# Performance work log

Measured on AMD Instinct MI355X. Metric: run time of the kernel, lower is better.

The kernel has to match this reference:

```python
import jax, jax.numpy as jnp
import numpy as np

T, HEADS, DIM_HEAD = 16, 16, 72
M = HEADS * DIM_HEAD  # 1152
SCALE = DIM_HEAD ** -0.5


def _ln(x, eps):
    mu = x.mean(-1, keepdims=True)
    var = x.var(-1, keepdims=True)
    return (x - mu) / jnp.sqrt(var + eps)


def _rotate_half(t):
    # interleaved pairs (x1, x2) -> (-x2, x1), as in rotary-embedding-torch
    t1, t2 = t[..., 0::2], t[..., 1::2]
    return jnp.stack([-t2, t1], axis=-1).reshape(t.shape)


def _rotary(t, pos):
    d = t.shape[-1]
    inv_freq = 1.0 / (10000.0 ** (jnp.arange(0, d, 2, dtype=jnp.float32) / d))
    freqs = pos.astype(jnp.float32)[:, None] * inv_freq          # (T, d/2)
    freqs = jnp.repeat(freqs, 2, axis=-1)                        # (T, d)
    return t * jnp.cos(freqs) + _rotate_half(t) * jnp.sin(freqs)


def _forward(x, c4t, c, W_ada, b_ada, tn_w, tn_b, t_qkv, t_k, t_v, t_out,
             t_fc_w, t_fc_b, s_qkv, s_k, s_v, s_out,
             mlp_w1, mlp_b1, mlp_w2, mlp_b2, f):
    B = c4t.shape[0]
    K, N, _ = x.shape

    ada = jax.nn.silu(c4t) @ W_ada + b_ada                       # (B, 6M)
    sh_msa, sc_msa, g_msa, sh_mlp, sc_mlp, g_mlp = jnp.split(ada, 6, axis=1)

    x4 = x.reshape(B, T, N, M)

    # ---- temporal attention (seq dim = frames, rotary, per-frame cond k/v) ----
    xt = _ln(x4, 1e-5) * tn_w + tn_b                             # temporal_norm1
    xt = xt.transpose(0, 2, 1, 3)                                # (B, N, T, M)
    q, k, v = jnp.split(xt @ t_qkv, 3, axis=-1)

    def heads_t(t):  # (B,N,T,M) -> (B,N,h,T,d)
        return t.reshape(B, N, T, HEADS, DIM_HEAD).transpose(0, 1, 3, 2, 4)

    q, k, v = map(heads_t, (q, k, v))
    k = _rotary(k, f)
    ek = (c @ t_k).reshape(B, T, HEADS, DIM_HEAD).transpose(0, 2, 1, 3)  # (B,h,T,d)
    ev = (c @ t_v).reshape(B, T, HEADS, DIM_HEAD).transpose(0, 2, 1, 3)
    ek = _rotary(ek, f)
    ek = jnp.broadcast_to(ek[:, None], k.shape)                  # (B,N,h,T,d)
    ev = jnp.broadcast_to(ev[:, None], v.shape)
    kk = jnp.concatenate([ek, k], axis=-2)                       # (B,N,h,2T,d)
    vv = jnp.concatenate([ev, v], axis=-2)
    q = _rotary(q * SCALE, f)
    attn = jax.nn.softmax(jnp.einsum('bnhid,bnhjd->bnhij', q, kk), axis=-1)
    out = jnp.einsum('bnhij,bnhjd->bnhid', attn, vv)
    out = out.transpose(0, 1, 3, 2, 4).reshape(B, N, T, M) @ t_out
    res = out.transpose(0, 2, 1, 3) @ t_fc_w + t_fc_b            # (B,T,N,M)
    x4 = x4 + res

    # ---- spatial attention with adaLN modulate + one cond token per frame ----
    mod = _ln(x4, 1e-6) * (1.0 + sc_msa[:, None, None, :]) + sh_msa[:, None, None, :]
    q, k, v = jnp.split(mod @ s_qkv, 3, axis=-1)

    def heads_s(t):  # (B,T,N,M) -> (B,T,h,N,d)
        return t.reshape(B, T, N, HEADS, DIM_HEAD).transpose(0, 1, 3, 2, 4)

    q, k, v = map(heads_s, (q, k, v))
    ek = (c @ s_k).reshape(B, T, HEADS, DIM_HEAD)[:, :, :, None, :]  # (B,T,h,1,d)
    ev = (c @ s_v).reshape(B, T, HEADS, DIM_HEAD)[:, :, :, None, :]
    kk = jnp.concatenate([ek, k], axis=-2)                       # (B,T,h,N+1,d)
    vv = jnp.concatenate([ev, v], axis=-2)
    attn = jax.nn.softmax(jnp.einsum('bthid,bthjd->bthij', q * SCALE, kk), axis=-1)
    out = jnp.einsum('bthij,bthjd->bthid', attn, vv)
    out = out.transpose(0, 1, 3, 2, 4).reshape(B, T, N, M) @ s_out
    x4 = x4 + g_msa[:, None, None, :] * out

    # ---- gated MLP with adaLN modulate ----
    mod2 = _ln(x4, 1e-6) * (1.0 + sc_mlp[:, None, None, :]) + sh_mlp[:, None, None, :]
    h = jax.nn.gelu(mod2 @ mlp_w1 + mlp_b1, approximate=True)
    y = h @ mlp_w2 + mlp_b2
    x4 = x4 + g_mlp[:, None, None, :] * y
    return x4.reshape(K, N, M)


def setup_inputs() -> dict:
    key = jax.random.key(0)
    ks = jax.random.split(key, 20)
    B, N = 2, 256

    def w(k, shape, s=0.02):
        return jax.random.normal(k, shape, jnp.float32) * s

    return {
        'x': jax.random.normal(ks[0], (B * T, N, M), jnp.float32),
        'c4t': jax.random.normal(ks[1], (B, M), jnp.float32),
        'c': jax.random.normal(ks[2], (B, T, M), jnp.float32),
        'W_ada': w(ks[3], (M, 6 * M)), 'b_ada': w(ks[4], (6 * M,)),
        'tn_w': jnp.ones(M, jnp.float32), 'tn_b': jnp.zeros(M, jnp.float32),
        't_qkv': w(ks[5], (M, 3 * M)), 't_k': w(ks[6], (M, M)),
        't_v': w(ks[7], (M, M)), 't_out': w(ks[8], (M, M)),
        't_fc_w': w(ks[9], (M, M)), 't_fc_b': jnp.zeros(M, jnp.float32),
        's_qkv': w(ks[10], (M, 3 * M)), 's_k': w(ks[11], (M, M)),
        's_v': w(ks[12], (M, M)), 's_out': w(ks[13], (M, M)),
        'mlp_w1': w(ks[14], (M, 4 * M)), 'mlp_b1': jnp.zeros(4 * M, jnp.float32),
        'mlp_w2': w(ks[15], (4 * M, M)), 'mlp_b2': jnp.zeros(M, jnp.float32),
        'f': jnp.arange(T, dtype=jnp.int32),
    }


def reference(x, c4t, c, W_ada, b_ada, tn_w, tn_b, t_qkv, t_k, t_v, t_out,
              t_fc_w, t_fc_b, s_qkv, s_k, s_v, s_out,
              mlp_w1, mlp_b1, mlp_w2, mlp_b2, f):
    return _forward(x, c4t, c, W_ada, b_ada, tn_w, tn_b, t_qkv, t_k, t_v, t_out,
                    t_fc_w, t_fc_b, s_qkv, s_k, s_v, s_out,
                    mlp_w1, mlp_b1, mlp_w2, mlp_b2, f)
```

## Files before the change

### kernel.cpp

```cpp
#include <hip/hip_runtime.h>
#include <hip/hip_bf16.h>

typedef __hip_bfloat16 bf16;
typedef __attribute__((ext_vector_type(8))) short short8;
typedef __attribute__((ext_vector_type(4))) float floatx4;

__device__ __forceinline__ float b2f(bf16 v) { return __bfloat162float(v); }
__device__ __forceinline__ short f2bs(float v) {
    bf16 h = __float2bfloat16(v);
    return *(short*)&h;
}
__device__ __forceinline__ float invfreq(int jj) {
    return expf(-0.25584278811044955f * (float)jj);
}

template<int MODE>
__device__ __forceinline__ float ldin(const void* p, long i) {
    if (MODE == 0) return b2f(((const bf16*)p)[i]);
    else           return ((const float*)p)[i];
}
__device__ __forceinline__ float ldf(const void* p, long i, int fl) {
    return fl == 0 ? b2f(((const bf16*)p)[i]) : ((const float*)p)[i];
}

#define SCALE_ 0.11785113019775793f

#define GLDS(gp, lp) __builtin_amdgcn_global_load_lds( \
    (const __attribute__((address_space(1))) void*)(gp), \
    (__attribute__((address_space(3))) void*)(lp), 16, 0, 0)

__global__ void k_detect(const void* __restrict__ x, int* __restrict__ flag)
{
    const unsigned short* u = (const unsigned short*)x;
    int tid = threadIdx.x;
    int insane = 0;
    for (int i = tid; i < 2048; i += 64) {
        unsigned short s = u[i];
        int ex = (s >> 7) & 0xFF;
        if (ex >= 0xC5) insane++;
    }
    #pragma unroll
    for (int off = 32; off > 0; off >>= 1) insane += __shfl_down(insane, off);
    if (tid == 0) flag[0] = (insane > 8) ? 1 : 0;
}

__global__ void k_setup(const void* __restrict__ c4t, const void* __restrict__ c,
                        const void* __restrict__ t_fcb, const void* __restrict__ mlp_b1,
                        const void* __restrict__ mlp_b2, const int* __restrict__ f,
                        float* __restrict__ sc4, float* __restrict__ cf32,
                        float* __restrict__ fcb_f, float* __restrict__ b1_f,
                        float* __restrict__ b2_f, float* __restrict__ ropeC,
                        float* __restrict__ ropeS, const int* __restrict__ flg)
{
    int i = blockIdx.x * 256 + threadIdx.x;
    int fl = *flg;
    if (i < 2304) {
        float v = ldf(c4t, i, fl);
        sc4[i] = v / (1.f + expf(-v));
    } else if (i < 39168) {
        cf32[i - 2304] = ldf(c, i - 2304, fl);
    } else if (i < 40320) {
        fcb_f[i - 39168] = ldf(t_fcb, i - 39168, fl);
    } else if (i < 44928) {
        b1_f[i - 40320] = ldf(mlp_b1, i - 40320, fl);
    } else if (i < 46080) {
        b2_f[i - 44928] = ldf(mlp_b2, i - 44928, fl);
    } else if (i < 47232) {
        int idx = i - 46080;
        int t = idx / 72, d = idx - t * 72;
        float ang = (float)f[t] * invfreq(d >> 1);
        float sn, cs; sincosf(ang, &sn, &cs);
        ropeC[idx] = cs;
        ropeS[idx] = sn;
    }
}

__global__ void k_cvtb(const float* __restrict__ in, bf16* __restrict__ out, int n)
{
    int i = blockIdx.x * 256 + threadIdx.x;
    if (i < n) out[i] = __float2bfloat16(in[i]);
}

template<int MODE>
__device__ __forceinline__ void wt_body(float (*tile)[33], const void* __restrict__ W,
    bf16* __restrict__ Wt, int K, int N)
{
    int n0 = blockIdx.x << 5, k0 = blockIdx.y << 5;
    int tid = threadIdx.x;
    int r = tid >> 3, c4 = (tid & 7) << 2;
    long base = (long)(k0 + r) * N + n0 + c4;
    #pragma unroll
    for (int i = 0; i < 4; ++i) tile[r][c4 + i] = ldin<MODE>(W, base + i);
    __syncthreads();
    long obase = (long)(n0 + r) * K + k0 + c4;
    #pragma unroll
    for (int i = 0; i < 4; ++i) Wt[obase + i] = __float2bfloat16(tile[c4 + i][r]);
}

__global__ __launch_bounds__(256) void k_wt(const void* __restrict__ W,
    bf16* __restrict__ Wt, int K, int N, const int* __restrict__ flg)
{
    __shared__ float tile[32][33];
    if (*flg == 0) wt_body<0>(tile, W, Wt, K, N);
    else           wt_body<1>(tile, W, Wt, K, N);
}

__global__ __launch_bounds__(256) void k_wt2(const void* __restrict__ W0,
    const void* __restrict__ W1, bf16* __restrict__ Wt0, const int* __restrict__ flg)
{
    __shared__ float tile[32][33];
    const void* W = blockIdx.z ? W1 : W0;
    bf16* Wt = Wt0 + (long)blockIdx.z * 3981312;
    if (*flg == 0) wt_body<0>(tile, W, Wt, 1152, 3456);
    else           wt_body<1>(tile, W, Wt, 1152, 3456);
}

__global__ __launch_bounds__(256) void k_wt3(const void* __restrict__ W0,
    const void* __restrict__ W1, const void* __restrict__ W2,
    bf16* __restrict__ Wt0, const int* __restrict__ flg)
{
    __shared__ float tile[32][33];
    const void* W = (blockIdx.z == 0) ? W0 : (blockIdx.z == 1) ? W1 : W2;
    bf16* Wt = Wt0 + (long)blockIdx.z * 1327104;
    if (*flg == 0) wt_body<0>(tile, W, Wt, 1152, 1152);
    else           wt_body<1>(tile, W, Wt, 1152, 1152);
}

template<int MODE>
__device__ __forceinline__ void gemm_body(
    float (*As)[64], float (*Bs)[64],
    const float* __restrict__ A, const void* __restrict__ W,
    const void* __restrict__ bias, float* __restrict__ C,
    int row0, int R, int K, int N)
{
    int tid = threadIdx.x;
    int tx = tid & 15, ty = tid >> 4;
    int col0 = blockIdx.x << 6;
    float acc[4][4] = {};
    int ar = tid >> 2;
    int ak = (tid & 3) << 2;
    int bk = tid >> 4;
    int bc = (tid & 15) << 2;
    for (int kt = 0; kt < K; kt += 16) {
        if (row0 + ar < R) {
            const float4 a4 = *(const float4*)(A + (long)(row0 + ar) * K + kt + ak);
            As[ak + 0][ar] = a4.x; As[ak + 1][ar] = a4.y;
            As[ak + 2][ar] = a4.z; As[ak + 3][ar] = a4.w;
        } else {
            As[ak + 0][ar] = 0.f; As[ak + 1][ar] = 0.f;
            As[ak + 2][ar] = 0.f; As[ak + 3][ar] = 0.f;
        }
        #pragma unroll
        for (int i = 0; i < 4; ++i)
            Bs[bk][bc + i] = ldin<MODE>(W, (long)(kt + bk) * N + col0 + bc + i);
        __syncthreads();
        #pragma unroll
        for (int kk = 0; kk < 16; ++kk) {
            float4 av = *(const float4*)&As[kk][ty << 2];
            float4 bv = *(const float4*)&Bs[kk][tx << 2];
            float a[4] = {av.x, av.y, av.z, av.w};
            float b[4] = {bv.x, bv.y, bv.z, bv.w};
            #pragma unroll
            for (int i = 0; i < 4; ++i)
                #pragma unroll
                for (int j = 0; j < 4; ++j)
                    acc[i][j] += a[i] * b[j];
        }
        __syncthreads();
    }
    #pragma unroll
    for (int i = 0; i < 4; ++i) {
        int gr = row0 + (ty << 2) + i;
        if (gr >= R) continue;
        float* cp = C + (long)gr * N + col0 + (tx << 2);
        #pragma unroll
        for (int j = 0; j < 4; ++j) {
            float v = acc[i][j];
            if (bias) v += ldin<MODE>(bias, col0 + (tx << 2) + j);
            cp[j] = v;
        }
    }
}

__global__ __launch_bounds__(256) void k_gemm(
    const float* __restrict__ A, const void* __restrict__ W,
    const void* __restrict__ bias, float* __restrict__ C,
    int R, int K, int N, const int* __restrict__ flg)
{
    __shared__ float As[16][64];
    __shared__ float Bs[16][64];
    if (*flg == 0) gemm_body<0>(As, Bs, A, W, bias, C, (int)(blockIdx.y << 6), R, K, N);
    else           gemm_body<1>(As, Bs, A, W, bias, C, (int)(blockIdx.y << 6), R, K, N);
}

__global__ __launch_bounds__(256) void k_gemm4(
    const float* __restrict__ A, const void* __restrict__ W0,
    const void* __restrict__ W1, const void* __restrict__ W2,
    const void* __restrict__ W3, float* __restrict__ C0,
    const int* __restrict__ flg)
{
    __shared__ float As[16][64];
    __shared__ float Bs[16][64];
    int z = blockIdx.y;
    const void* W = (z == 0) ? W0 : (z == 1) ? W1 : (z == 2) ? W2 : W3;
    float* C = C0 + (long)z * 36864;
    if (*flg == 0) gemm_body<0>(As, Bs, A, W, nullptr, C, 0, 32, 1152, 1152);
    else           gemm_body<1>(As, Bs, A, W, nullptr, C, 0, 32, 1152, 1152);
}

template<int EMODE>
__global__ __launch_bounds__(256, 3) void k_mgemm(
    const bf16* __restrict__ A, const bf16* __restrict__ Wt,
    const float* __restrict__ bias, void* __restrict__ Cout,
    int K, int N, int outbf, int act,
    float* __restrict__ x4, const float* __restrict__ ada, int part,
    const void* __restrict__ xin, void* __restrict__ outp,
    const int* __restrict__ flg)
{
    __shared__ short As[12288];
    __shared__ short Bs[12288];
    int tid = threadIdx.x;
    int lane = tid & 63, wave = tid >> 6;
    int mq = wave >> 1, nq = wave & 1;

    int gx = gridDim.x;
    int nwg = gx * (int)gridDim.y;
    int orig = blockIdx.y * gx + blockIdx.x;
    int qq = nwg >> 3, rr = nwg & 7;
    int xcd = orig & 7, loc = orig >> 3;
    int wg = (xcd < rr ? xcd * (qq + 1) : rr * (qq + 1) + (xcd - rr) * qq) + loc;
    int bx = wg % gx, by = wg / gx;

    long row0 = (long)by << 7;
    long col0 = (long)bx << 7;
    int mi = lane & 15, q = lane >> 4;

    const bf16* gA0 = A  + (row0 + (2 * wave) * 16 + mi) * K + q * 8;
    const bf16* gA1 = gA0 + 16 * K;
    const bf16* gB0 = Wt + (col0 + (2 * wave) * 16 + mi) * K + q * 8;
    const bf16* gB1 = gB0 + 16 * K;
    int dA0 = (2 * wave) * 512, dA1 = dA0 + 512;

    floatx4 acc[4][4] = {};
    int nt = K >> 5;

    GLDS(gA0,      &As[dA0]);
    GLDS(gA1,      &As[dA1]);
    GLDS(gB0,      &Bs[dA0]);
    GLDS(gB1,      &Bs[dA1]);
    GLDS(gA0 + 32, &As[4096 + dA0]);
    GLDS(gA1 + 32, &As[4096 + dA1]);
    GLDS(gB0 + 32, &Bs[4096 + dA0]);
    GLDS(gB1 + 32, &Bs[4096 + dA1]);
    __builtin_amdgcn_sched_barrier(0);
    asm volatile("s_waitcnt vmcnt(4)" ::: "memory");
    __builtin_amdgcn_sched_barrier(0);
    __builtin_amdgcn_s_barrier();
    __builtin_amdgcn_sched_barrier(0);

    int aRd = mq * 2048 + lane * 8;
    int bRd = nq * 2048 + lane * 8;
    int cs = 0;
    int si = 2;

    for (int t = 0; t < nt; ++t) {
        if (t + 2 < nt) {
            int o = si << 12;
            int kt2 = (t + 2) << 5;
            GLDS(gA0 + kt2, &As[o + dA0]);
            GLDS(gA1 + kt2, &As[o + dA1]);
            GLDS(gB0 + kt2, &Bs[o + dA0]);
            GLDS(gB1 + kt2, &Bs[o + dA1]);
        }
        {
            int o = cs << 12;
            short8 af[4], bfr[4];
            #pragma unroll
            for (int i = 0; i < 4; ++i)
                af[i] = *(const short8*)&As[o + aRd + i * 512];
            #pragma unroll
            for (int j = 0; j < 4; ++j)
                bfr[j] = *(const short8*)&Bs[o + bRd + j * 512];
            #pragma unroll
            for (int i = 0; i < 4; ++i)
                #pragma unroll
                for (int j = 0; j < 4; ++j)
                    acc[i][j] = __builtin_amdgcn_mfma_f32_16x16x32_bf16(
                        af[i], bfr[j], acc[i][j], 0, 0, 0);
        }
        __builtin_amdgcn_sched_barrier(0);
        if (t + 2 < nt) asm volatile("s_waitcnt vmcnt(4)" ::: "memory");
        else            asm volatile("s_waitcnt vmcnt(0)" ::: "memory");
        __builtin_amdgcn_sched_barrier(0);
        if (t < nt - 1) {
            __builtin_amdgcn_s_barrier();
            __builtin_amdgcn_sched_barrier(0);
        }
        cs = (cs == 2) ? 0 : cs + 1;
        si = (si == 2) ? 0 : si + 1;
    }

    int lr = lane >> 4, lc = lane & 15;
    int fl = flg ? *flg : 0;
    float b4[4] = {0.f, 0.f, 0.f, 0.f};
    if (bias) {
        #pragma unroll
        for (int j = 0; j < 4; ++j) b4[j] = bias[(int)col0 + nq * 64 + j * 16 + lc];
    }
    #pragma unroll
    for (int i = 0; i < 4; ++i) {
        #pragma unroll
        for (int r = 0; r < 4; ++r) {
            long grow = row0 + mq * 64 + i * 16 + lr * 4 + r;
            #pragma unroll
            for (int j = 0; j < 4; ++j) {
                int col = (int)col0 + nq * 64 + j * 16 + lc;
                float v = acc[i][j][r] + b4[j];
                if (act) {
                    float u = v;
                    float tt = 1.5957691216057308f * (u + 0.044715f * u * u * u);
                    v = u / (1.f + __expf(-tt));
                }
                if constexpr (EMODE == 0) {
                    if (outbf) ((bf16*)Cout)[grow * N + col] = __float2bfloat16(v);
                    else       ((float*)Cout)[grow * N + col] = v;
                } else if constexpr (EMODE == 1) {
                    int bb = (int)(grow >> 12);
                    int nn = ((int)grow >> 4) & 255;
                    int tt2 = (int)grow & 15;
                    long rx = ((long)((bb << 4) + tt2) << 8) + nn;
                    long idx = rx * 1152 + col;
                    float xv = (fl == 0) ? b2f(((const bf16*)xin)[idx])
                                         : ((const float*)xin)[idx];
                    x4[idx] = xv + v;
                } else {
                    int bb = (int)(grow >> 12);
                    float g = ada[(bb * 6 + part) * 1152 + col];
                    long idx = grow * 1152 + col;
                    float nv = x4[idx] + g * v;
                    x4[idx] = nv;
                    if (outp) {
                        if (fl == 0) ((bf16*)outp)[idx] = __float2bfloat16(nv);
                        else         ((float*)outp)[idx] = nv;
                    }
                }
            }
        }
    }
}

template<int MODE>
__device__ __forceinline__ void ln_t_body(float* rs, float* rss,
    const void* __restrict__ x, const void* __restrict__ w,
    const void* __restrict__ bb, bf16* __restrict__ out)
{
    int r = blockIdx.x;
    int n = r & 255;
    int bt = r >> 8;
    int b = bt >> 4, t = bt & 15;
    long orow = (long)((b << 8) + n) * 16 + t;
    int tid = threadIdx.x;
    float vals[5];
    float s = 0.f, ss = 0.f;
    int c = 0;
    for (int i = tid; i < 1152; i += 256, ++c) {
        float v = ldin<MODE>(x, (long)r * 1152 + i);
        vals[c] = v; s += v; ss += v * v;
    }
    #pragma unroll
    for (int off = 32; off > 0; off >>= 1) {
        s  += __shfl_down(s, off);
        ss += __shfl_down(ss, off);
    }
    int wid = tid >> 6;
    if ((tid & 63) == 0) { rs[wid] = s; rss[wid] = ss; }
    __syncthreads();
    float S  = rs[0] + rs[1] + rs[2] + rs[3];
    float SS = rss[0] + rss[1] + rss[2] + rss[3];
    float mu = S * (1.f / 1152.f);
    float var = SS * (1.f / 1152.f) - mu * mu;
    float rstd = rsqrtf(var + 1e-5f);
    c = 0;
    bf16* op = out + orow * 1152;
    for (int i = tid; i < 1152; i += 256, ++c)
        op[i] = __float2bfloat16((vals[c] - mu) * rstd * ldin<MODE>(w, i) + ldin<MODE>(bb, i));
}

__global__ __launch_bounds__(256) void k_ln_t(
    const void* __restrict__ x, const void* __restrict__ w,
    const void* __restrict__ bb, bf16* __restrict__ out,
    const int* __restrict__ flg)
{
    __shared__ float rs[4], rss[4];
    if (*flg == 0) ln_t_body<0>(rs, rss, x, w, bb, out);
    else           ln_t_body<1>(rs, rss, x, w, bb, out);
}

__global__ __launch_bounds__(256) void k_ln_mod(
    const float* __restrict__ x4, const float* __restrict__ ada,
    int psh, int psc, float eps, bf16* __restrict__ out)
{
    int r = blockIdx.x;
    int b = r >> 12;
    const float* xp = x4 + (long)r * 1152;
    int tid = threadIdx.x;
    float vals[5];
    float s = 0.f, ss = 0.f;
    int c = 0;
    for (int i = tid; i < 1152; i += 256, ++c) {
        float v = xp[i];
        vals[c] = v; s += v; ss += v * v;
    }
    #pragma unroll
    for (int off = 32; off > 0; off >>= 1) {
        s  += __shfl_down(s, off);
        ss += __shfl_down(ss, off);
    }
    __shared__ float rs[4], rss[4];
    int wid = tid >> 6;
    if ((tid & 63) == 0) { rs[wid] = s; rss[wid] = ss; }
    __syncthreads();
    float S  = rs[0] + rs[1] + rs[2] + rs[3];
    float SS = rss[0] + rss[1] + rss[2] + rss[3];
    float mu = S * (1.f / 1152.f);
    float var = SS * (1.f / 1152.f) - mu * mu;
    float rstd = rsqrtf(var + eps);
    const float* sh = ada + (b * 6 + psh) * 1152;
    const float* sc = ada + (b * 6 + psc) * 1152;
    c = 0;
    bf16* op = out + (long)r * 1152;
    for (int i = tid; i < 1152; i += 256, ++c)
        op[i] = __float2bfloat16((vals[c] - mu) * rstd * (1.f + sc[i]) + sh[i]);
}

__global__ __launch_bounds__(256) void k_attn_t(
    const bf16* __restrict__ qkv, const float* __restrict__ ekt,
    const float* __restrict__ evt, const float* __restrict__ ropeC,
    const float* __restrict__ ropeS, bf16* __restrict__ out)
{
    __shared__ float qs[16][73];
    __shared__ float ksT[72][33];
    __shared__ float vs[32][73];
    __shared__ float sc[16][33];
    int blk = blockIdx.x;
    int h = blk & 15;
    int bn = blk >> 4;
    int b = bn >> 8;
    int tid = threadIdx.x;
    long qbase = (long)bn * 16 * 3456 + h * 72;
    for (int idx = tid; idx < 16 * 72; idx += 256) {
        int i = idx / 72, d = idx - i * 72;
        long p0 = qbase + (long)i * 3456;
        float v  = b2f(qkv[p0 + d]);
        float v2 = b2f(qkv[p0 + (d ^ 1)]);
        float cs = ropeC[idx], sn = ropeS[idx];
        float rv = (d & 1) ? (v * cs + v2 * sn) : (v * cs - v2 * sn);
        qs[i][d] = rv * SCALE_;
    }
    for (int idx = tid; idx < 32 * 72; idx += 256) {
        int j = idx / 72, d = idx - j * 72;
        float kv, kv2, vv; int pi;
        if (j < 16) {
            long base = (long)(b * 16 + j) * 1152 + h * 72;
            kv  = ekt[base + d];
            kv2 = ekt[base + (d ^ 1)];
            vv  = evt[base + d];
            pi = j;
        } else {
            int jj = j - 16;
            long base = qbase + (long)jj * 3456;
            kv  = b2f(qkv[base + 1152 + d]);
            kv2 = b2f(qkv[base + 1152 + (d ^ 1)]);
            vv  = b2f(qkv[base + 2304 + d]);
            pi = jj;
        }
        float cs = ropeC[pi * 72 + d], sn = ropeS[pi * 72 + d];
        ksT[d][j] = (d & 1) ? (kv * cs + kv2 * sn) : (kv * cs - kv2 * sn);
        vs[j][d] = vv;
    }
    __syncthreads();
    for (int e = tid; e < 512; e += 256) {
        int i = e >> 5, j = e & 31;
        float s = 0.f;
        for (int d = 0; d < 72; ++d) s += qs[i][d] * ksT[d][j];
        sc[i][j] = s;
    }
    __syncthreads();
    if (tid < 16) {
        float m = -1e30f;
        for (int j = 0; j < 32; ++j) m = fmaxf(m, sc[tid][j]);
        float l = 0.f;
        for (int j = 0; j < 32; ++j) { float p = expf(sc[tid][j] - m); sc[tid][j] = p; l += p; }
        float inv = 1.f / l;
        for (int j = 0; j < 32; ++j) sc[tid][j] *= inv;
    }
    __syncthreads();
    for (int idx = tid; idx < 16 * 72; idx += 256) {
        int i = idx / 72, d = idx - i * 72;
        float o = 0.f;
        for (int j = 0; j < 32; ++j) o += sc[i][j] * vs[j][d];
        out[((long)bn * 16 + i) * 1152 + h * 72 + d] = __float2bfloat16(o);
    }
}

__global__ __launch_bounds__(256) void k_attn_s(
    const bf16* __restrict__ qkv, const bf16* __restrict__ eksb,
    const bf16* __restrict__ evsb, bf16* __restrict__ out)
{
    __shared__ short vT[5120];
    __shared__ short pl[4][1024];
    int tid = threadIdx.x;
    int lane = tid & 63, wave = tid >> 6;
    int blk = blockIdx.x;
    int ic = blk & 3;
    int bth = blk >> 2;
    int h = bth & 15;
    int bt = bth >> 4;
    int col = lane & 15, q = lane >> 4;
    int hoff = h * 72;
    long qkvbase = (long)bt * 256 * 3456;
    long ctxbase = (long)bt * 1152 + hoff;

    int qrow = ic * 64 + wave * 16 + col;
    const bf16* qptr = qkv + qkvbase + (long)qrow * 3456 + hoff;
    short8 qf[3];
    #pragma unroll
    for (int ks = 0; ks < 3; ++ks) {
        int k0 = ks * 32 + q * 8;
        if (k0 + 8 <= 72) qf[ks] = *(const short8*)(qptr + k0);
        else { short8 z = {0,0,0,0,0,0,0,0}; qf[ks] = z; }
    }

    floatx4 o[5] = {};
    float m_i[4], l_i[4];
    #pragma unroll
    for (int r = 0; r < 4; ++r) { m_i[r] = -1e30f; l_i[r] = 0.f; }

    for (int kc = 0; kc < 320; kc += 64) {
        for (int fi = tid; fi < 640; fi += 256) {
            int blkid = fi >> 6, fl2 = fi & 63;
            int dn = blkid >> 1, ks = blkid & 1;
            int d = dn * 16 + (fl2 & 15);
            int kq = fl2 >> 4;
            short8 v;
            #pragma unroll
            for (int j = 0; j < 8; ++j) {
                int gk = kc + ks * 32 + kq * 8 + j;
                short sv = 0;
                if (d < 72 && gk <= 256) {
                    if (gk == 0) sv = *(const short*)(eksb ? &evsb[ctxbase + d] : nullptr);
                    else sv = *(const short*)&qkv[qkvbase + (long)(gk - 1) * 3456 + 2304 + hoff + d];
                }
                v[j] = sv;
            }
            *(short8*)&vT[blkid * 512 + fl2 * 8] = v;
        }
        __syncthreads();

        floatx4 sacc[4] = {};
        #pragma unroll
        for (int nt = 0; nt < 4; ++nt) {
            int key = kc + nt * 16 + col;
            #pragma unroll
            for (int ks = 0; ks < 3; ++ks) {
                int k0 = ks * 32 + q * 8;
                short8 kf = {0,0,0,0,0,0,0,0};
                if (key <= 256 && k0 + 8 <= 72) {
                    if (key == 0) kf = *(const short8*)(eksb + ctxbase + k0);
                    else kf = *(const short8*)(qkv + qkvbase + (long)(key - 1) * 3456 + 1152 + hoff + k0);
                }
                sacc[nt] = __builtin_amdgcn_mfma_f32_16x16x32_bf16(qf[ks], kf, sacc[nt], 0, 0, 0);
            }
        }

        float p[4][4];
        #pragma unroll
        for (int r = 0; r < 4; ++r) {
            float mv = -1e30f;
            #pragma unroll
            for (int nt = 0; nt < 4; ++nt) {
                int key = kc + nt * 16 + col;
                float s = (key <= 256) ? sacc[nt][r] * SCALE_ : -1e30f;
                p[nt][r] = s;
                mv = fmaxf(mv, s);
            }
            #pragma unroll
            for (int xm = 1; xm < 16; xm <<= 1) mv = fmaxf(mv, __shfl_xor(mv, xm));
            float mn = fmaxf(m_i[r], mv);
            float alpha = expf(m_i[r] - mn);
            m_i[r] = mn;
            float rsum = 0.f;
            #pragma unroll
            for (int nt = 0; nt < 4; ++nt) {
                float e = expf(p[nt][r] - mn);
                p[nt][r] = e;
                rsum += e;
            }
            #pragma unroll
            for (int xm = 1; xm < 16; xm <<= 1) rsum += __shfl_xor(rsum, xm);
            l_i[r] = l_i[r] * alpha + rsum;
            #pragma unroll
            for (int dn = 0; dn < 5; ++dn) o[dn][r] *= alpha;
        }

        #pragma unroll
        for (int nt = 0; nt < 4; ++nt) {
            int kl = nt * 16 + col;
            int ks2 = kl >> 5, q2 = (kl >> 3) & 3, j = kl & 7;
            #pragma unroll
            for (int r = 0; r < 4; ++r) {
                int mrow = q * 4 + r;
                pl[wave][ks2 * 512 + q2 * 128 + mrow * 8 + j] = f2bs(p[nt][r]);
            }
        }
        __syncthreads();

        #pragma unroll
        for (int ks = 0; ks < 2; ++ks) {
            short8 pf = *(const short8*)&pl[wave][ks * 512 + lane * 8];
            #pragma unroll
            for (int dn = 0; dn < 5; ++dn) {
                short8 vf = *(const short8*)&vT[(dn * 2 + ks) * 512 + lane * 8];
                o[dn] = __builtin_amdgcn_mfma_f32_16x16x32_bf16(pf, vf, o[dn], 0, 0, 0);
            }
        }
        __syncthreads();
    }

    int orow0 = ic * 64 + wave * 16;
    #pragma unroll
    for (int dn = 0; dn < 5; ++dn) {
        int d = dn * 16 + col;
        if (d >= 72) continue;
        #pragma unroll
        for (int r = 0; r < 4; ++r) {
            int mrow = q * 4 + r;
            float val = o[dn][r] / l_i[r];
            out[((long)bt * 256 + orow0 + mrow) * 1152 + hoff + d] = __float2bfloat16(val);
        }
    }
}

extern "C" void kernel_launch(void* const* d_in, const int* in_sizes, int n_in,
                              void* d_out, int out_size, void* d_ws, size_t ws_size,
                              hipStream_t stream)
{
    const void* x      = d_in[0];
    const void* c4t    = d_in[1];
    const void* c      = d_in[2];
    const void* W_ada  = d_in[3];
    const void* b_ada  = d_in[4];
    const void* tn_w   = d_in[5];
    const void* tn_b   = d_in[6];
    const void* t_qkv  = d_in[7];
    const void* t_k    = d_in[8];
    const void* t_v    = d_in[9];
    const void* t_outw = d_in[10];
    const void* t_fcw  = d_in[11];
    const void* t_fcb  = d_in[12];
    const void* s_qkv  = d_in[13];
    const void* s_k    = d_in[14];
    const void* s_v    = d_in[15];
    const void* s_outw = d_in[16];
    const void* mlp_w1 = d_in[17];
    const void* mlp_b1 = d_in[18];
    const void* mlp_w2 = d_in[19];
    const void* mlp_b2 = d_in[20];
    const int*  f      = (const int*)d_in[21];

    float* ws    = (float*)d_ws;
    float* x4    = ws;
    float* buf2  = x4 + 9437184;
    float* reg1f = buf2 + 9437184;
    bf16*  qkvb  = (bf16*)reg1f;
    bf16*  hbf   = (bf16*)reg1f;
    float* abfAf = reg1f + 18874368;
    bf16*  abfA  = (bf16*)abfAf;
    float* abfBf = abfAf + 4718592;
    bf16*  abfB  = (bf16*)abfBf;
    float* wtf   = abfBf + 4718592;
    bf16*  wt    = (bf16*)wtf;
    bf16* t_qkv_t = wt;
    bf16* s_qkv_t = t_qkv_t + 3981312;
    bf16* t_out_t = s_qkv_t + 3981312;
    bf16* t_fc_t  = t_out_t + 1327104;
    bf16* s_out_t = t_fc_t  + 1327104;
    bf16* w1_t    = s_out_t + 1327104;
    bf16* w2_t    = w1_t    + 5308416;
    float* small  = wtf + 11280384;
    float* ada   = small;
    float* cf32  = ada  + 13824;
    float* ekt   = cf32 + 36864;
    float* evt   = ekt  + 36864;
    float* eks   = evt  + 36864;
    float* evs   = eks  + 36864;
    bf16*  eksb  = (bf16*)(evs + 36864);
    bf16*  evsb  = eksb + 36864;
    float* sc4   = (float*)(evsb + 36864);
    float* fcb_f = sc4  + 2304;
    float* b1_f  = fcb_f + 1152;
    float* b2_f  = b1_f  + 4608;
    float* ropeC = b2_f + 1152;
    float* ropeS = ropeC + 1152;
    int*   flg   = (int*)(ropeS + 1152);

    k_detect<<<1, 64, 0, stream>>>(x, flg);
    k_setup<<<185, 256, 0, stream>>>(c4t, c, t_fcb, mlp_b1, mlp_b2, f,
                                     sc4, cf32, fcb_f, b1_f, b2_f, ropeC, ropeS, flg);

    k_gemm<<<dim3(108, 1), 256, 0, stream>>>(sc4, W_ada, b_ada, ada, 2, 1152, 6912, flg);
    k_gemm4<<<dim3(18, 4), 256, 0, stream>>>(cf32, t_k, t_v, s_k, s_v, ekt, flg);
    k_cvtb<<<288, 256, 0, stream>>>(eks, eksb, 73728);

    k_wt2<<<dim3(108, 36, 2), 256, 0, stream>>>(t_qkv, s_qkv, t_qkv_t, flg);
    k_wt3<<<dim3(36, 36, 3), 256, 0, stream>>>(t_outw, t_fcw, s_outw, t_out_t, flg);
    k_wt<<<dim3(144, 36), 256, 0, stream>>>(mlp_w1, w1_t, 1152, 4608, flg);
    k_wt<<<dim3(36, 144), 256, 0, stream>>>(mlp_w2, w2_t, 4608, 1152, flg);

    k_ln_t<<<8192, 256, 0, stream>>>(x, tn_w, tn_b, abfA, flg);
    k_mgemm<0><<<dim3(27, 64), 256, 0, stream>>>(abfA, t_qkv_t, nullptr, qkvb, 1152, 3456, 1, 0,
                                                 nullptr, nullptr, 0, nullptr, nullptr, flg);
    k_attn_t<<<8192, 256, 0, stream>>>(qkvb, ekt, evt, ropeC, ropeS, abfB);
    k_mgemm<0><<<dim3(9, 64), 256, 0, stream>>>(abfB, t_out_t, nullptr, abfA, 1152, 1152, 1, 0,
                                                nullptr, nullptr, 0, nullptr, nullptr, flg);
    k_mgemm<1><<<dim3(9, 64), 256, 0, stream>>>(abfA, t_fc_t, fcb_f, nullptr, 1152, 1152, 0, 0,
                                                x4, nullptr, 0, x, nullptr, flg);

    k_ln_mod<<<8192, 256, 0, stream>>>(x4, ada, 0, 1, 1e-6f, abfA);
    k_mgemm<0><<<dim3(27, 64), 256, 0, stream>>>(abfA, s_qkv_t, nullptr, qkvb, 1152, 3456, 1, 0,
                                                 nullptr, nullptr, 0, nullptr, nullptr, flg);
    k_attn_s<<<2048, 256, 0, stream>>>(qkvb, eksb, evsb, abfB);
    k_mgemm<2><<<dim3(9, 64), 256, 0, stream>>>(abfB, s_out_t, nullptr, nullptr, 1152, 1152, 0, 0,
                                                x4, ada, 2, nullptr, nullptr, flg);

    k_ln_mod<<<8192, 256, 0, stream>>>(x4, ada, 3, 4, 1e-6f, abfA);
    k_mgemm<0><<<dim3(36, 64), 256, 0, stream>>>(abfA, w1_t, b1_f, hbf, 1152, 4608, 1, 1,
                                                 nullptr, nullptr, 0, nullptr, nullptr, flg);
    k_mgemm<2><<<dim3(9, 64), 256, 0, stream>>>(hbf, w2_t, b2_f, nullptr, 4608, 1152, 0, 0,
                                                x4, ada, 5, nullptr, d_out, flg);
}
```

Measured before the change: 1.487 ms.

## Load MFMA GEMM operands straight to registers and fuse bf16 conversion into gemm4

The main bf16 MFMA GEMM no longer stages tiles in LDS through a triple-buffered global_load_lds pipeline with barriers. Each wave now loads its own A and B fragments directly from global memory into registers, double-buffered across k-steps. This removes LDS traffic and block-wide syncs, but every wave re-reads operands that the other waves of the block share, so global and L2 traffic goes up. Separately, gemm4 writes the spatial k/v outputs directly as bf16, which removes the standalone conversion kernel launch.

After: 2.117 ms. 42.3% more time.

```diff
diff --git a/kernel.cpp b/kernel.cpp
--- a/kernel.cpp
+++ b/kernel.cpp
@@ -24,10 +24,6 @@
 }
 
 #define SCALE_ 0.11785113019775793f
-
-#define GLDS(gp, lp) __builtin_amdgcn_global_load_lds( \
-    (const __attribute__((address_space(1))) void*)(gp), \
-    (__attribute__((address_space(3))) void*)(lp), 16, 0, 0)
 
 __global__ void k_detect(const void* __restrict__ x, int* __restrict__ flag)
 {
@@ -75,12 +71,6 @@
     }
 }
 
-__global__ void k_cvtb(const float* __restrict__ in, bf16* __restrict__ out, int n)
-{
-    int i = blockIdx.x * 256 + threadIdx.x;
-    if (i < n) out[i] = __float2bfloat16(in[i]);
-}
-
 template<int MODE>
 __device__ __forceinline__ void wt_body(float (*tile)[33], const void* __restrict__ W,
     bf16* __restrict__ Wt, int K, int N)
@@ -131,7 +121,7 @@
     float (*As)[64], float (*Bs)[64],
     const float* __restrict__ A, const void* __restrict__ W,
     const void* __restrict__ bias, float* __restrict__ C,
-    int row0, int R, int K, int N)
+    bf16* __restrict__ Cb, int row0, int R, int K, int N)
 {
     int tid = threadIdx.x;
     int tx = tid & 15, ty = tid >> 4;
@@ -172,12 +162,13 @@
     for (int i = 0; i < 4; ++i) {
         int gr = row0 + (ty << 2) + i;
         if (gr >= R) continue;
-        float* cp = C + (long)gr * N + col0 + (tx << 2);
         #pragma unroll
         for (int j = 0; j < 4; ++j) {
             float v = acc[i][j];
-            if (bias) v += ldin<MODE>(bias, col0 + (tx << 2) + j);
-            cp[j] = v;
+            int cc = col0 + (tx << 2) + j;
+            if (bias) v += ldin<MODE>(bias, cc);
+            if (Cb) Cb[(long)gr * N + cc] = __float2bfloat16(v);
+            else    C[(long)gr * N + cc] = v;
         }
     }
 }
@@ -189,23 +180,24 @@
 {
     __shared__ float As[16][64];
     __shared__ float Bs[16][64];
-    if (*flg == 0) gemm_body<0>(As, Bs, A, W, bias, C, (int)(blockIdx.y << 6), R, K, N);
-    else           gemm_body<1>(As, Bs, A, W, bias, C, (int)(blockIdx.y << 6), R, K, N);
+    if (*flg == 0) gemm_body<0>(As, Bs, A, W, bias, C, nullptr, (int)(blockIdx.y << 6), R, K, N);
+    else           gemm_body<1>(As, Bs, A, W, bias, C, nullptr, (int)(blockIdx.y << 6), R, K, N);
 }
 
 __global__ __launch_bounds__(256) void k_gemm4(
     const float* __restrict__ A, const void* __restrict__ W0,
     const void* __restrict__ W1, const void* __restrict__ W2,
     const void* __restrict__ W3, float* __restrict__ C0,
-    const int* __restrict__ flg)
+    bf16* __restrict__ Cb0, const int* __restrict__ flg)
 {
     __shared__ float As[16][64];
     __shared__ float Bs[16][64];
     int z = blockIdx.y;
     const void* W = (z == 0) ? W0 : (z == 1) ? W1 : (z == 2) ? W2 : W3;
     float* C = C0 + (long)z * 36864;
-    if (*flg == 0) gemm_body<0>(As, Bs, A, W, nullptr, C, 0, 32, 1152, 1152);
-    else           gemm_body<1>(As, Bs, A, W, nullptr, C, 0, 32, 1152, 1152);
+    bf16* Cb = (z >= 2) ? Cb0 + (long)(z - 2) * 36864 : nullptr;
+    if (*flg == 0) gemm_body<0>(As, Bs, A, W, nullptr, C, Cb, 0, 32, 1152, 1152);
+    else           gemm_body<1>(As, Bs, A, W, nullptr, C, Cb, 0, 32, 1152, 1152);
 }
 
 template<int EMODE>
@@ -217,8 +209,6 @@
     const void* __restrict__ xin, void* __restrict__ outp,
     const int* __restrict__ flg)
 {
-    __shared__ short As[12288];
-    __shared__ short Bs[12288];
     int tid = threadIdx.x;
     int lane = tid & 63, wave = tid >> 6;
     int mq = wave >> 1, nq = wave & 1;
@@ -235,70 +225,47 @@
     long col0 = (long)bx << 7;
     int mi = lane & 15, q = lane >> 4;
 
-    const bf16* gA0 = A  + (row0 + (2 * wave) * 16 + mi) * K + q * 8;
-    const bf16* gA1 = gA0 + 16 * K;
-    const bf16* gB0 = Wt + (col0 + (2 * wave) * 16 + mi) * K + q * 8;
-    const bf16* gB1 = gB0 + 16 * K;
-    int dA0 = (2 * wave) * 512, dA1 = dA0 + 512;
+    const bf16* pa0 = A  + (row0 + mq * 64 + mi) * (long)K + q * 8;
+    const bf16* pa1 = pa0 + 16 * (long)K;
+    const bf16* pa2 = pa0 + 32 * (long)K;
+    const bf16* pa3 = pa0 + 48 * (long)K;
+    const bf16* pb0 = Wt + (col0 + nq * 64 + mi) * (long)K + q * 8;
+    const bf16* pb1 = pb0 + 16 * (long)K;
+    const bf16* pb2 = pb0 + 32 * (long)K;
+    const bf16* pb3 = pb0 + 48 * (long)K;
 
     floatx4 acc[4][4] = {};
     int nt = K >> 5;
 
-    GLDS(gA0,      &As[dA0]);
-    GLDS(gA1,      &As[dA1]);
-    GLDS(gB0,      &Bs[dA0]);
-    GLDS(gB1,      &Bs[dA1]);
-    GLDS(gA0 + 32, &As[4096 + dA0]);
-    GLDS(gA1 + 32, &As[4096 + dA1]);
-    GLDS(gB0 + 32, &Bs[4096 + dA0]);
-    GLDS(gB1 + 32, &Bs[4096 + dA1]);
-    __builtin_amdgcn_sched_barrier(0);
-    asm volatile("s_waitcnt vmcnt(4)" ::: "memory");
-    __builtin_amdgcn_sched_barrier(0);
-    __builtin_amdgcn_s_barrier();
-    __builtin_amdgcn_sched_barrier(0);
-
-    int aRd = mq * 2048 + lane * 8;
-    int bRd = nq * 2048 + lane * 8;
-    int cs = 0;
-    int si = 2;
-
-    for (int t = 0; t < nt; ++t) {
-        if (t + 2 < nt) {
-            int o = si << 12;
-            int kt2 = (t + 2) << 5;
-            GLDS(gA0 + kt2, &As[o + dA0]);
-            GLDS(gA1 + kt2, &As[o + dA1]);
-            GLDS(gB0 + kt2, &Bs[o + dA0]);
-            GLDS(gB1 + kt2, &Bs[o + dA1]);
-        }
-        {
-            int o = cs << 12;
-            short8 af[4], bfr[4];
-            #pragma unroll
-            for (int i = 0; i < 4; ++i)
-                af[i] = *(const short8*)&As[o + aRd + i * 512];
-            #pragma unroll
-            for (int j = 0; j < 4; ++j)
-                bfr[j] = *(const short8*)&Bs[o + bRd + j * 512];
-            #pragma unroll
-            for (int i = 0; i < 4; ++i)
-                #pragma unroll
-                for (int j = 0; j < 4; ++j)
-                    acc[i][j] = __builtin_amdgcn_mfma_f32_16x16x32_bf16(
-                        af[i], bfr[j], acc[i][j], 0, 0, 0);
-        }
-        __builtin_amdgcn_sched_barrier(0);
-        if (t + 2 < nt) asm volatile("s_waitcnt vmcnt(4)" ::: "memory");
-        else            asm volatile("s_waitcnt vmcnt(0)" ::: "memory");
-        __builtin_amdgcn_sched_barrier(0);
-        if (t < nt - 1) {
-            __builtin_amdgcn_s_barrier();
-            __builtin_amdgcn_sched_barrier(0);
-        }
-        cs = (cs == 2) ? 0 : cs + 1;
-        si = (si == 2) ? 0 : si + 1;
-    }
+    short8 a0[4], b0[4], a1[4], b1[4];
+
+#define LD8(dA, dB, kt) do { \
+        dA[0] = *(const short8*)(pa0 + (kt)); \
+        dA[1] = *(const short8*)(pa1 + (kt)); \
+        dA[2] = *(const short8*)(pa2 + (kt)); \
+        dA[3] = *(const short8*)(pa3 + (kt)); \
+        dB[0] = *(const short8*)(pb0 + (kt)); \
+        dB[1] = *(const short8*)(pb1 + (kt)); \
+        dB[2] = *(const short8*)(pb2 + (kt)); \
+        dB[3] = *(const short8*)(pb3 + (kt)); } while (0)
+
+#define MM16(sA, sB) do { \
+        _Pragma("unroll") \
+        for (int i_ = 0; i_ < 4; ++i_) \
+            _Pragma("unroll") \
+            for (int j_ = 0; j_ < 4; ++j_) \
+                acc[i_][j_] = __builtin_amdgcn_mfma_f32_16x16x32_bf16( \
+                    sA[i_], sB[j_], acc[i_][j_], 0, 0, 0); } while (0)
+
+    LD8(a0, b0, 0);
+    for (int t = 0; t < nt; t += 2) {
+        if (t + 1 < nt) LD8(a1, b1, (t + 1) * 32);
+        MM16(a0, b0);
+        if (t + 2 < nt) LD8(a0, b0, (t + 2) * 32);
+        if (t + 1 < nt) MM16(a1, b1);
+    }
+#undef LD8
+#undef MM16
 
     int lr = lane >> 4, lc = lane & 15;
     int fl = flg ? *flg : 0;
@@ -709,8 +676,7 @@
                                      sc4, cf32, fcb_f, b1_f, b2_f, ropeC, ropeS, flg);
 
     k_gemm<<<dim3(108, 1), 256, 0, stream>>>(sc4, W_ada, b_ada, ada, 2, 1152, 6912, flg);
-    k_gemm4<<<dim3(18, 4), 256, 0, stream>>>(cf32, t_k, t_v, s_k, s_v, ekt, flg);
-    k_cvtb<<<288, 256, 0, stream>>>(eks, eksb, 73728);
+    k_gemm4<<<dim3(18, 4), 256, 0, stream>>>(cf32, t_k, t_v, s_k, s_v, ekt, eksb, flg);
 
     k_wt2<<<dim3(108, 36, 2), 256, 0, stream>>>(t_qkv, s_qkv, t_qkv_t, flg);
     k_wt3<<<dim3(36, 36, 3), 256, 0, stream>>>(t_outw, t_fcw, s_outw, t_out_t, flg);
```

## Fold temporal out and fc projections into one weight, vectorize layernorms

Applied to the files above, without the earlier changes.

Precomputes the product of the temporal out-projection and fc weights with one small GEMM per call, so the two consecutive 1152x1152 GEMMs over all tokens become a single one. It also rewrites the layernorm kernels to use 320 threads with float4 or ushort4 vector loads and stores. The spatial-attention k/v conversion is fused into the gemm4 epilogue, which removes one launch. The folded weight is rounded to bf16, which changes numerics slightly, and the extra weight product adds a little per-call work.

Result: no change. 1.462 ms (-1.7%).

```diff
diff --git a/kernel.cpp b/kernel.cpp
--- a/kernel.cpp
+++ b/kernel.cpp
@@ -75,10 +75,11 @@
     }
 }
 
-__global__ void k_cvtb(const float* __restrict__ in, bf16* __restrict__ out, int n)
+__global__ void k_cvtf(const void* __restrict__ in, bf16* __restrict__ out, int n,
+                       const int* __restrict__ flg)
 {
     int i = blockIdx.x * 256 + threadIdx.x;
-    if (i < n) out[i] = __float2bfloat16(in[i]);
+    if (i < n) out[i] = __float2bfloat16(ldf(in, i, *flg));
 }
 
 template<int MODE>
@@ -131,7 +132,7 @@
     float (*As)[64], float (*Bs)[64],
     const float* __restrict__ A, const void* __restrict__ W,
     const void* __restrict__ bias, float* __restrict__ C,
-    int row0, int R, int K, int N)
+    bf16* __restrict__ Cb, int row0, int R, int K, int N)
 {
     int tid = threadIdx.x;
     int tx = tid & 15, ty = tid >> 4;
@@ -172,12 +173,13 @@
     for (int i = 0; i < 4; ++i) {
         int gr = row0 + (ty << 2) + i;
         if (gr >= R) continue;
-        float* cp = C + (long)gr * N + col0 + (tx << 2);
         #pragma unroll
         for (int j = 0; j < 4; ++j) {
             float v = acc[i][j];
-            if (bias) v += ldin<MODE>(bias, col0 + (tx << 2) + j);
-            cp[j] = v;
+            int cc = col0 + (tx << 2) + j;
+            if (bias) v += ldin<MODE>(bias, cc);
+            if (Cb) Cb[(long)gr * N + cc] = __float2bfloat16(v);
+            else    C[(long)gr * N + cc] = v;
         }
     }
 }
@@ -189,23 +191,24 @@
 {
     __shared__ float As[16][64];
     __shared__ float Bs[16][64];
-    if (*flg == 0) gemm_body<0>(As, Bs, A, W, bias, C, (int)(blockIdx.y << 6), R, K, N);
-    else           gemm_body<1>(As, Bs, A, W, bias, C, (int)(blockIdx.y << 6), R, K, N);
+    if (*flg == 0) gemm_body<0>(As, Bs, A, W, bias, C, nullptr, (int)(blockIdx.y << 6), R, K, N);
+    else           gemm_body<1>(As, Bs, A, W, bias, C, nullptr, (int)(blockIdx.y << 6), R, K, N);
 }
 
 __global__ __launch_bounds__(256) void k_gemm4(
     const float* __restrict__ A, const void* __restrict__ W0,
     const void* __restrict__ W1, const void* __restrict__ W2,
     const void* __restrict__ W3, float* __restrict__ C0,
-    const int* __restrict__ flg)
+    bf16* __restrict__ Cb0, const int* __restrict__ flg)
 {
     __shared__ float As[16][64];
     __shared__ float Bs[16][64];
     int z = blockIdx.y;
     const void* W = (z == 0) ? W0 : (z == 1) ? W1 : (z == 2) ? W2 : W3;
     float* C = C0 + (long)z * 36864;
-    if (*flg == 0) gemm_body<0>(As, Bs, A, W, nullptr, C, 0, 32, 1152, 1152);
-    else           gemm_body<1>(As, Bs, A, W, nullptr, C, 0, 32, 1152, 1152);
+    bf16* Cb = (z >= 2) ? Cb0 + (long)(z - 2) * 36864 : nullptr;
+    if (*flg == 0) gemm_body<0>(As, Bs, A, W, nullptr, C, Cb, 0, 32, 1152, 1152);
+    else           gemm_body<1>(As, Bs, A, W, nullptr, C, Cb, 0, 32, 1152, 1152);
 }
 
 template<int EMODE>
@@ -349,24 +352,34 @@
     }
 }
 
-template<int MODE>
-__device__ __forceinline__ void ln_t_body(float* rs, float* rss,
+__global__ __launch_bounds__(320) void k_ln_t(
     const void* __restrict__ x, const void* __restrict__ w,
-    const void* __restrict__ bb, bf16* __restrict__ out)
-{
+    const void* __restrict__ bb, bf16* __restrict__ out,
+    const int* __restrict__ flg)
+{
+    __shared__ float rs[5], rss[5];
     int r = blockIdx.x;
     int n = r & 255;
     int bt = r >> 8;
     int b = bt >> 4, t = bt & 15;
     long orow = (long)((b << 8) + n) * 16 + t;
     int tid = threadIdx.x;
-    float vals[5];
-    float s = 0.f, ss = 0.f;
-    int c = 0;
-    for (int i = tid; i < 1152; i += 256, ++c) {
-        float v = ldin<MODE>(x, (long)r * 1152 + i);
-        vals[c] = v; s += v; ss += v * v;
-    }
+    int fl = *flg;
+    float4 v4 = make_float4(0.f, 0.f, 0.f, 0.f);
+    int c0 = tid << 2;
+    if (tid < 288) {
+        if (fl == 0) {
+            ushort4 u = *(const ushort4*)((const unsigned short*)x + (long)r * 1152 + c0);
+            bf16 h0, h1, h2, h3;
+            *(unsigned short*)&h0 = u.x; *(unsigned short*)&h1 = u.y;
+            *(unsigned short*)&h2 = u.z; *(unsigned short*)&h3 = u.w;
+            v4 = make_float4(b2f(h0), b2f(h1), b2f(h2), b2f(h3));
+        } else {
+            v4 = *(const float4*)((const float*)x + (long)r * 1152 + c0);
+        }
+    }
+    float s  = v4.x + v4.y + v4.z + v4.w;
+    float ss = v4.x * v4.x + v4.y * v4.y + v4.z * v4.z + v4.w * v4.w;
     #pragma unroll
     for (int off = 32; off > 0; off >>= 1) {
         s  += __shfl_down(s, off);
@@ -375,62 +388,62 @@
     int wid = tid >> 6;
     if ((tid & 63) == 0) { rs[wid] = s; rss[wid] = ss; }
     __syncthreads();
-    float S  = rs[0] + rs[1] + rs[2] + rs[3];
-    float SS = rss[0] + rss[1] + rss[2] + rss[3];
+    float S  = rs[0] + rs[1] + rs[2] + rs[3] + rs[4];
+    float SS = rss[0] + rss[1] + rss[2] + rss[3] + rss[4];
     float mu = S * (1.f / 1152.f);
     float var = SS * (1.f / 1152.f) - mu * mu;
     float rstd = rsqrtf(var + 1e-5f);
-    c = 0;
-    bf16* op = out + orow * 1152;
-    for (int i = tid; i < 1152; i += 256, ++c)
-        op[i] = __float2bfloat16((vals[c] - mu) * rstd * ldin<MODE>(w, i) + ldin<MODE>(bb, i));
-}
-
-__global__ __launch_bounds__(256) void k_ln_t(
-    const void* __restrict__ x, const void* __restrict__ w,
-    const void* __restrict__ bb, bf16* __restrict__ out,
-    const int* __restrict__ flg)
-{
-    __shared__ float rs[4], rss[4];
-    if (*flg == 0) ln_t_body<0>(rs, rss, x, w, bb, out);
-    else           ln_t_body<1>(rs, rss, x, w, bb, out);
-}
-
-__global__ __launch_bounds__(256) void k_ln_mod(
+    if (tid < 288) {
+        ushort4 o4;
+        float w0 = ldf(w, c0, fl),     w1 = ldf(w, c0 + 1, fl);
+        float w2 = ldf(w, c0 + 2, fl), w3 = ldf(w, c0 + 3, fl);
+        float bb0 = ldf(bb, c0, fl),     bb1 = ldf(bb, c0 + 1, fl);
+        float bb2 = ldf(bb, c0 + 2, fl), bb3 = ldf(bb, c0 + 3, fl);
+        o4.x = (unsigned short)f2bs((v4.x - mu) * rstd * w0 + bb0);
+        o4.y = (unsigned short)f2bs((v4.y - mu) * rstd * w1 + bb1);
+        o4.z = (unsigned short)f2bs((v4.z - mu) * rstd * w2 + bb2);
+        o4.w = (unsigned short)f2bs((v4.w - mu) * rstd * w3 + bb3);
+        *(ushort4*)((unsigned short*)out + orow * 1152 + c0) = o4;
+    }
+}
+
+__global__ __launch_bounds__(320) void k_ln_mod(
     const float* __restrict__ x4, const float* __restrict__ ada,
     int psh, int psc, float eps, bf16* __restrict__ out)
 {
+    __shared__ float rs[5], rss[5];
     int r = blockIdx.x;
     int b = r >> 12;
     const float* xp = x4 + (long)r * 1152;
     int tid = threadIdx.x;
-    float vals[5];
-    float s = 0.f, ss = 0.f;
-    int c = 0;
-    for (int i = tid; i < 1152; i += 256, ++c) {
-        float v = xp[i];
-        vals[c] = v; s += v; ss += v * v;
-    }
+    int c0 = tid << 2;
+    float4 v4 = make_float4(0.f, 0.f, 0.f, 0.f);
+    if (tid < 288) v4 = *(const float4*)(xp + c0);
+    float s  = v4.x + v4.y + v4.z + v4.w;
+    float ss = v4.x * v4.x + v4.y * v4.y + v4.z * v4.z + v4.w * v4.w;
     #pragma unroll
     for (int off = 32; off > 0; off >>= 1) {
         s  += __shfl_down(s, off);
         ss += __shfl_down(ss, off);
     }
-    __shared__ float rs[4], rss[4];
     int wid = tid >> 6;
     if ((tid & 63) == 0) { rs[wid] = s; rss[wid] = ss; }
     __syncthreads();
-    float S  = rs[0] + rs[1] + rs[2] + rs[3];
-    float SS = rss[0] + rss[1] + rss[2] + rss[3];
+    float S  = rs[0] + rs[1] + rs[2] + rs[3] + rs[4];
+    float SS = rss[0] + rss[1] + rss[2] + rss[3] + rss[4];
     float mu = S * (1.f / 1152.f);
     float var = SS * (1.f / 1152.f) - mu * mu;
     float rstd = rsqrtf(var + eps);
-    const float* sh = ada + (b * 6 + psh) * 1152;
-    const float* sc = ada + (b * 6 + psc) * 1152;
-    c = 0;
-    bf16* op = out + (long)r * 1152;
-    for (int i = tid; i < 1152; i += 256, ++c)
-        op[i] = __float2bfloat16((vals[c] - mu) * rstd * (1.f + sc[i]) + sh[i]);
+    if (tid < 288) {
+        float4 sh4 = *(const float4*)(ada + (b * 6 + psh) * 1152 + c0);
+        float4 sc4 = *(const float4*)(ada + (b * 6 + psc) * 1152 + c0);
+        ushort4 o4;
+        o4.x = (unsigned short)f2bs((v4.x - mu) * rstd * (1.f + sc4.x) + sh4.x);
+        o4.y = (unsigned short)f2bs((v4.y - mu) * rstd * (1.f + sc4.y) + sh4.y);
+        o4.z = (unsigned short)f2bs((v4.z - mu) * rstd * (1.f + sc4.z) + sh4.z);
+        o4.w = (unsigned short)f2bs((v4.w - mu) * rstd * (1.f + sc4.w) + sh4.w);
+        *(ushort4*)((unsigned short*)out + (long)r * 1152 + c0) = o4;
+    }
 }
 
 __global__ __launch_bounds__(256) void k_attn_t(
@@ -671,6 +684,8 @@
     float* ws    = (float*)d_ws;
     float* x4    = ws;
     float* buf2  = x4 + 9437184;
+    bf16*  wc_t  = (bf16*)buf2;
+    bf16*  t_out_b = wc_t + 1327104;
     float* reg1f = buf2 + 9437184;
     bf16*  qkvb  = (bf16*)reg1f;
     bf16*  hbf   = (bf16*)reg1f;
@@ -709,31 +724,32 @@
                                      sc4, cf32, fcb_f, b1_f, b2_f, ropeC, ropeS, flg);
 
     k_gemm<<<dim3(108, 1), 256, 0, stream>>>(sc4, W_ada, b_ada, ada, 2, 1152, 6912, flg);
-    k_gemm4<<<dim3(18, 4), 256, 0, stream>>>(cf32, t_k, t_v, s_k, s_v, ekt, flg);
-    k_cvtb<<<288, 256, 0, stream>>>(eks, eksb, 73728);
+    k_gemm4<<<dim3(18, 4), 256, 0, stream>>>(cf32, t_k, t_v, s_k, s_v, ekt, eksb, flg);
 
     k_wt2<<<dim3(108, 36, 2), 256, 0, stream>>>(t_qkv, s_qkv, t_qkv_t, flg);
     k_wt3<<<dim3(36, 36, 3), 256, 0, stream>>>(t_outw, t_fcw, s_outw, t_out_t, flg);
     k_wt<<<dim3(144, 36), 256, 0, stream>>>(mlp_w1, w1_t, 1152, 4608, flg);
     k_wt<<<dim3(36, 144), 256, 0, stream>>>(mlp_w2, w2_t, 4608, 1152, flg);
 
-    k_ln_t<<<8192, 256, 0, stream>>>(x, tn_w, tn_b, abfA, flg);
+    k_cvtf<<<5184, 256, 0, stream>>>(t_outw, t_out_b, 1327104, flg);
+    k_mgemm<0><<<dim3(9, 9), 256, 0, stream>>>(t_fc_t, t_out_b, nullptr, wc_t, 1152, 1152, 1, 0,
+                                               nullptr, nullptr, 0, nullptr, nullptr, flg);
+
+    k_ln_t<<<8192, 320, 0, stream>>>(x, tn_w, tn_b, abfA, flg);
     k_mgemm<0><<<dim3(27, 64), 256, 0, stream>>>(abfA, t_qkv_t, nullptr, qkvb, 1152, 3456, 1, 0,
                                                  nullptr, nullptr, 0, nullptr, nullptr, flg);
     k_attn_t<<<8192, 256, 0, stream>>>(qkvb, ekt, evt, ropeC, ropeS, abfB);
-    k_mgemm<0><<<dim3(9, 64), 256, 0, stream>>>(abfB, t_out_t, nullptr, abfA, 1152, 1152, 1, 0,
-                                                nullptr, nullptr, 0, nullptr, nullptr, flg);
-    k_mgemm<1><<<dim3(9, 64), 256, 0, stream>>>(abfA, t_fc_t, fcb_f, nullptr, 1152, 1152, 0, 0,
+    k_mgemm<1><<<dim3(9, 64), 256, 0, stream>>>(abfB, wc_t, fcb_f, nullptr, 1152, 1152, 0, 0,
                                                 x4, nullptr, 0, x, nullptr, flg);
 
-    k_ln_mod<<<8192, 256, 0, stream>>>(x4, ada, 0, 1, 1e-6f, abfA);
+    k_ln_mod<<<8192, 320, 0, stream>>>(x4, ada, 0, 1, 1e-6f, abfA);
     k_mgemm<0><<<dim3(27, 64), 256, 0, stream>>>(abfA, s_qkv_t, nullptr, qkvb, 1152, 3456, 1, 0,
                                                  nullptr, nullptr, 0, nullptr, nullptr, flg);
     k_attn_s<<<2048, 256, 0, stream>>>(qkvb, eksb, evsb, abfB);
     k_mgemm<2><<<dim3(9, 64), 256, 0, stream>>>(abfB, s_out_t, nullptr, nullptr, 1152, 1152, 0, 0,
                                                 x4, ada, 2, nullptr, nullptr, flg);
 
-    k_ln_mod<<<8192, 256, 0, stream>>>(x4, ada, 3, 4, 1e-6f, abfA);
+    k_ln_mod<<<8192, 320, 0, stream>>>(x4, ada, 3, 4, 1e-6f, abfA);
     k_mgemm<0><<<dim3(36, 64), 256, 0, stream>>>(abfA, w1_t, b1_f, hbf, 1152, 4608, 1, 1,
                                                  nullptr, nullptr, 0, nullptr, nullptr, flg);
     k_mgemm<2><<<dim3(9, 64), 256, 0, stream>>>(hbf, w2_t, b2_f, nullptr, 4608, 1152, 0, 0,
```
